# Kernel optimization log

Hardware: AMD Instinct MI355X
Metric: run time of the kernel (lower is better)

The kernel has to match this reference:

```python
import jax, jax.numpy as jnp
import numpy as np

CLASSES = 21
IOU_THRESH = 0.5
ALPHA = 0.25   # focal loss alpha
GAMMA = 2.0    # focal loss gamma
SL1_BETA = 1.0 # torch SmoothL1Loss default beta
CLS_W = 1.0
REG_W = 1.0
NUM_ANCHORS = 98304
NUM_TARGETS = 1024


def _compute_iou(boxes_a, boxes_b):
    # boxes_a: [T,4], boxes_b: [A,4] in (x1,y1,x2,y2) -> [T,A]
    lt = jnp.maximum(boxes_a[:, None, :2], boxes_b[None, :, :2])
    rb = jnp.minimum(boxes_a[:, None, 2:], boxes_b[None, :, 2:])
    wh = jnp.clip(rb - lt, 0.0)
    inter = wh[..., 0] * wh[..., 1]
    area_a = (boxes_a[:, 2] - boxes_a[:, 0]) * (boxes_a[:, 3] - boxes_a[:, 1])
    area_b = (boxes_b[:, 2] - boxes_b[:, 0]) * (boxes_b[:, 3] - boxes_b[:, 1])
    union = area_a[:, None] + area_b[None, :] - inter
    return inter / jnp.maximum(union, 1e-8)


def _encode(boxes, anchors):
    bw = boxes[:, 2] - boxes[:, 0]
    bh = boxes[:, 3] - boxes[:, 1]
    bcx = boxes[:, 0] + 0.5 * bw
    bcy = boxes[:, 1] + 0.5 * bh
    aw = anchors[:, 2] - anchors[:, 0]
    ah = anchors[:, 3] - anchors[:, 1]
    acx = anchors[:, 0] + 0.5 * aw
    acy = anchors[:, 1] + 0.5 * ah
    tx = (bcx - acx) / aw
    ty = (bcy - acy) / ah
    tw = jnp.log(jnp.maximum(bw, 1e-8) / aw)
    th = jnp.log(jnp.maximum(bh, 1e-8) / ah)
    return jnp.stack([tx, ty, tw, th], axis=1)


def _focal_loss(logits, targets):
    # elementwise sigmoid focal loss (no reduction)
    p = jax.nn.sigmoid(logits)
    # numerically stable BCE with logits
    ce = jnp.maximum(logits, 0.0) - logits * targets + jnp.log1p(jnp.exp(-jnp.abs(logits)))
    p_t = p * targets + (1.0 - p) * (1.0 - targets)
    alpha_t = ALPHA * targets + (1.0 - ALPHA) * (1.0 - targets)
    return alpha_t * (1.0 - p_t) ** GAMMA * ce


def _smooth_l1(diff):
    ad = jnp.abs(diff)
    return jnp.where(ad < SL1_BETA, 0.5 * diff * diff / SL1_BETA, ad - 0.5 * SL1_BETA)


def setup_inputs() -> dict:
    key = jax.random.key(0)
    kA, kW, kT, kJ, kL, kC, kB = jax.random.split(key, 7)
    A, T = NUM_ANCHORS, NUM_TARGETS
    centers = jax.random.uniform(kA, (A, 2), minval=0.15, maxval=0.85)
    sizes = jax.random.uniform(kW, (A, 2), minval=0.05, maxval=0.30)
    anchors = jnp.concatenate([centers - 0.5 * sizes, centers + 0.5 * sizes], axis=1)
    # targets = jittered anchors so IoU >= 0.5 matches exist
    idx = jax.random.randint(kT, (T,), 0, A)
    jitter = jax.random.uniform(kJ, (T, 4), minval=-0.01, maxval=0.01)
    target_boxes = anchors[idx] + jitter
    target_labels = jax.random.randint(kL, (T,), 0, CLASSES)
    classification_preds = jax.random.normal(kC, (A, CLASSES), dtype=jnp.float32)
    boxes_preds = jax.random.normal(kB, (A, 4), dtype=jnp.float32)
    return {
        'classification_preds': classification_preds,
        'boxes_preds': boxes_preds,
        'anchors': anchors,
        'target_boxes': target_boxes,
        'target_labels': target_labels,
    }


def reference(classification_preds, boxes_preds, anchors, target_boxes, target_labels):
    iou = _compute_iou(target_boxes, anchors)  # [T, A]

    # anchor-side matching -> classification targets
    max_iou_for_anchors = jnp.max(iou, axis=0)          # [A]
    target_ids_for_anchors = jnp.argmax(iou, axis=0)     # [A]
    positive_mask = max_iou_for_anchors >= IOU_THRESH    # [A] bool
    n_pos = jnp.sum(positive_mask.astype(jnp.float32))
    onehot = jax.nn.one_hot(target_labels[target_ids_for_anchors], CLASSES, dtype=jnp.float32)
    cls_targets = jnp.where(positive_mask[:, None], onehot, 0.0)
    cls_loss = jnp.sum(_focal_loss(classification_preds, cls_targets)) / n_pos

    max_iou_for_targets = jnp.max(iou, axis=1)          # [T]
    anchor_ids_for_targets = jnp.argmax(iou, axis=1)     # [T]
    t_mask = (max_iou_for_targets >= IOU_THRESH).astype(jnp.float32)  # [T]
    matched_anchors = anchors[anchor_ids_for_targets]    # [T,4]
    encoded = _encode(target_boxes, matched_anchors)     # [T,4]
    pred = boxes_preds[anchor_ids_for_targets]           # [T,4]
    diff = (pred - encoded) * t_mask[:, None]
    n_match = jnp.maximum(jnp.sum(t_mask), 1.0)
    reg_loss = jnp.sum(_smooth_l1(diff)) / (n_match * 4.0)  # mean over matched elements

    w_cls = cls_loss * CLS_W
    w_reg = reg_loss * REG_W
    return (w_cls + w_reg, w_cls, w_reg)
```

## Files before the change

### kernel.cpp

```cpp
#include <hip/hip_runtime.h>
#include <stdint.h>

#define NA 98304
#define NT 1024
#define NC 21
#define ACH 192
#define TCH 8
#define NBLK (ACH * TCH)
#define EPB  256
#define HI_MIN 0xBF000000u


__device__ __forceinline__ float f0(float x) {
    const float ax = fabsf(x);
    const float u  = __expf(-ax);
    const float ce = fmaxf(x, 0.f) + __logf(1.f + u);
    const float p  = (x >= 0.f ? 1.f : u) / (1.f + u);
    return 0.75f * p * p * ce;
}
__device__ __forceinline__ float f1(float x) {
    const float ax = fabsf(x);
    const float u  = __expf(-ax);
    const float ce = fmaxf(x, 0.f) - x + __logf(1.f + u);
    const float p  = (x >= 0.f ? 1.f : u) / (1.f + u);
    const float q  = 1.f - p;
    return 0.25f * q * q * ce;
}
__device__ __forceinline__ unsigned long long mk_key(float iou, unsigned int idx) {
    return ((unsigned long long)(__float_as_uint(iou) | 0x80000000u) << 32) |
           (unsigned long long)(0xFFFFFFFFu - idx);
}
__device__ __forceinline__ float smooth_l1(float d) {
    const float ad = fabsf(d);
    return (ad < 1.f) ? 0.5f * d * d : ad - 0.5f;
}

__global__ __launch_bounds__(256) void k_match(
    const float4* __restrict__ anchors,
    const float4* __restrict__ tboxes,
    const float4* __restrict__ preds4,
    unsigned long long* __restrict__ akeys,
    unsigned long long* __restrict__ tkeys,
    float* __restrict__ f0_part,
    unsigned* __restrict__ hdr)
{
    __shared__ float4 s_t[128];
    __shared__ unsigned long long s_tk[128];
    __shared__ float s_f[4];

    const int tid   = threadIdx.x;
    const int L     = blockIdx.y * ACH + blockIdx.x;
    const int tbase = blockIdx.y * 128;
    const int a0    = blockIdx.x * 512 + tid;
    const int a1    = a0 + 256;

    if (L == 0 && tid < 160) hdr[tid] = 0u;

    if (tid < 128) {
        s_t[tid]  = tboxes[tbase + tid];
        s_tk[tid] = 0ull;
    }
    const float4 A0 = anchors[a0];
    const float4 A1 = anchors[a1];

    float facc;
    {
        const int pb = L * 336;
        const float4 v0 = preds4[pb + tid];
        facc = (f0(v0.x) + f0(v0.y)) + (f0(v0.z) + f0(v0.w));
        if (tid < 80) {
            const float4 v1 = preds4[pb + 256 + tid];
            facc += (f0(v1.x) + f0(v1.y)) + (f0(v1.z) + f0(v1.w));
        }
    }
    __syncthreads();

    const float ar0 = (A0.z - A0.x) * (A0.w - A0.y);
    const float ar1 = (A1.z - A1.x) * (A1.w - A1.y);

    float b0 = 0.f, b1 = 0.f;
    int   i0 = -1,  i1 = -1;

    #pragma unroll 4
    for (int t = 0; t < 128; ++t) {
        const float4 tb = s_t[t];
        const float sa = (tb.z - tb.x) * (tb.w - tb.y);
        {
            const float lx = fmaxf(A0.x, tb.x);
            const float ly = fmaxf(A0.y, tb.y);
            const float rx = fminf(A0.z, tb.z);
            const float ry = fminf(A0.w, tb.w);
            const float w  = fmaxf(rx - lx, 0.f);
            const float h  = fmaxf(ry - ly, 0.f);
            const float inter = w * h;
            const float uni = (ar0 + sa) - inter;
            if (__builtin_expect(inter + inter >= uni, 0)) {
                const float iou = inter / uni;
                if (iou > b0) { b0 = iou; i0 = t; }
                atomicMax(&s_tk[t], mk_key(iou, (unsigned int)a0));
            }
        }
        {
            const float lx = fmaxf(A1.x, tb.x);
            const float ly = fmaxf(A1.y, tb.y);
            const float rx = fminf(A1.z, tb.z);
            const float ry = fminf(A1.w, tb.w);
            const float w  = fmaxf(rx - lx, 0.f);
            const float h  = fmaxf(ry - ly, 0.f);
            const float inter = w * h;
            const float uni = (ar1 + sa) - inter;
            if (__builtin_expect(inter + inter >= uni, 0)) {
                const float iou = inter / uni;
                if (iou > b1) { b1 = iou; i1 = t; }
                atomicMax(&s_tk[t], mk_key(iou, (unsigned int)a1));
            }
        }
    }

    if (i0 >= 0) atomicMax(&akeys[a0], mk_key(b0, (unsigned int)(tbase + i0)));
    if (i1 >= 0) atomicMax(&akeys[a1], mk_key(b1, (unsigned int)(tbase + i1)));

    for (int o = 32; o > 0; o >>= 1) facc += __shfl_down(facc, o);
    const int lane = tid & 63, wid = tid >> 6;
    if (lane == 0) s_f[wid] = facc;

    __syncthreads();
    if (tid < 128) {
        const unsigned long long tk = s_tk[tid];
        if (tk != 0ull) atomicMax(&tkeys[tbase + tid], tk);
    }
    if (tid == 0) f0_part[L] = s_f[0] + s_f[1] + s_f[2] + s_f[3];
}

__global__ __launch_bounds__(256) void k_epi(
    const float* __restrict__ preds,
    const int* __restrict__ tlabels,
    const float4* __restrict__ anchors,
    const float4* __restrict__ tboxes,
    const float4* __restrict__ bpreds,
    const unsigned long long* __restrict__ akeys,
    const unsigned long long* __restrict__ tkeys,
    const float* __restrict__ f0_part,
    double* __restrict__ loss_part,
    int* __restrict__ n_part,
    int* __restrict__ done,
    float* __restrict__ out)
{
    __shared__ float s_red[4];
    __shared__ int   s_cnt[4];
    __shared__ int   s_flag;
    __shared__ float s_s[4], s_m[4];
    __shared__ double s_dbl[64];
    __shared__ int    s_int[16];

    const int tid = threadIdx.x;
    const int blk = blockIdx.x;
    const int lane = tid & 63, wid = tid >> 6;

    float acc = 0.f;
    int   cnt = 0;
    {
        const int a = blk * 384 + tid;
        const unsigned long long k = akeys[a];
        if ((unsigned int)(k >> 32) >= HI_MIN) {
            cnt = 1;
            const int lab = tlabels[0xFFFFFFFFu - (unsigned int)k];
            acc += f1(preds[a * NC + lab]) - f0(preds[a * NC + lab]);
        }
    }
    if (tid < 128) {
        const int a = blk * 384 + 256 + tid;
        const unsigned long long k = akeys[a];
        if ((unsigned int)(k >> 32) >= HI_MIN) {
            cnt += 1;
            const int lab = tlabels[0xFFFFFFFFu - (unsigned int)k];
            acc += f1(preds[a * NC + lab]) - f0(preds[a * NC + lab]);
        }
    }
    if (tid < 6) acc += f0_part[blk * 6 + tid];

    for (int o = 32; o > 0; o >>= 1) {
        acc += __shfl_down(acc, o);
        cnt += __shfl_down(cnt, o);
    }
    if (lane == 0) { s_red[wid] = acc; s_cnt[wid] = cnt; }
    __syncthreads();
    if (tid == 0) {
        atomicAdd(&loss_part[blk & 63],
                  (double)(s_red[0] + s_red[1] + s_red[2] + s_red[3]));
        atomicAdd(&n_part[blk & 15], s_cnt[0] + s_cnt[1] + s_cnt[2] + s_cnt[3]);
        __threadfence();
        s_flag = (atomicAdd(done, 1) == EPB - 1);
    }
    __syncthreads();
    if (!s_flag) return;

    float s = 0.f, m = 0.f;
    #pragma unroll
    for (int j = 0; j < 4; ++j) {
        const int t = tid + 256 * j;
        const unsigned long long key = tkeys[t];
        if ((unsigned int)(key >> 32) >= HI_MIN) {
            const unsigned int ga = 0xFFFFFFFFu - (unsigned int)key;
            const float4 tb  = tboxes[t];
            const float4 abx = anchors[ga];
            const float4 pb  = bpreds[ga];
            const float bw = tb.z - tb.x, bh = tb.w - tb.y;
            const float bcx = tb.x + 0.5f * bw, bcy = tb.y + 0.5f * bh;
            const float aw = abx.z - abx.x, ah = abx.w - abx.y;
            const float acx = abx.x + 0.5f * aw, acy = abx.y + 0.5f * ah;
            const float tx = (bcx - acx) / aw;
            const float ty = (bcy - acy) / ah;
            const float tw = logf(fmaxf(bw, 1e-8f) / aw);
            const float th = logf(fmaxf(bh, 1e-8f) / ah);
            s += smooth_l1(pb.x - tx) + smooth_l1(pb.y - ty) +
                 smooth_l1(pb.z - tw) + smooth_l1(pb.w - th);
            m += 1.f;
        }
    }
    for (int o = 32; o > 0; o >>= 1) {
        s += __shfl_down(s, o);
        m += __shfl_down(m, o);
    }
    __syncthreads();
    if (lane == 0) { s_s[wid] = s; s_m[wid] = m; }

    if (tid < 64) s_dbl[tid] = atomicAdd(&loss_part[tid], 0.0);
    if (tid >= 64 && tid < 80) s_int[tid - 64] = atomicAdd(&n_part[tid - 64], 0);
    __syncthreads();
    if (tid == 0) {
        double cl = 0.0;
        for (int i = 0; i < 64; ++i) cl += s_dbl[i];
        int np = 0;
        for (int i = 0; i < 16; ++i) np += s_int[i];
        const float rs = s_s[0] + s_s[1] + s_s[2] + s_s[3];
        const float rm = s_m[0] + s_m[1] + s_m[2] + s_m[3];
        const float cls = (float)(cl / (double)np);
        const float reg = rs / (fmaxf(rm, 1.f) * 4.f);
        out[0] = cls + reg;
        out[1] = cls;
        out[2] = reg;
    }
}

extern "C" void kernel_launch(void* const* d_in, const int* in_sizes, int n_in,
                              void* d_out, int out_size, void* d_ws, size_t ws_size,
                              hipStream_t stream) {
    const float*  preds   = (const float*)d_in[0];
    const float4* preds4  = (const float4*)d_in[0];
    const float4* bpreds  = (const float4*)d_in[1];
    const float4* anchors = (const float4*)d_in[2];
    const float4* tboxes  = (const float4*)d_in[3];
    const int*    tlabels = (const int*)d_in[4];

    char* ws = (char*)d_ws;
    int*    done      = (int*)(ws + 0);
    double* loss_part = (double*)(ws + 64);
    int*    n_part    = (int*)(ws + 576);
    float*  f0_part   = (float*)(ws + 1024);
    unsigned long long* tkeys = (unsigned long long*)(ws + 8192);
    unsigned long long* akeys = (unsigned long long*)(ws + 16384);

    k_match<<<dim3(ACH, TCH), 256, 0, stream>>>(anchors, tboxes, preds4,
                                                akeys, tkeys, f0_part,
                                                (unsigned*)d_ws);
    k_epi<<<EPB, 256, 0, stream>>>(preds, tlabels, anchors, tboxes, bpreds,
                                   akeys, tkeys, f0_part, loss_part, n_part,
                                   done, (float*)d_out);
}
```

Before: 138.2 us.

## Fuse matching and epilogue into one kernel with last-block reductions

Merges the separate matching and epilogue kernels into a single launch. The last of the TCH target-chunk blocks for each anchor chunk computes the positive-anchor correction and count. The last of those per-chunk finishers then does the target-side regression and the final reduction. This removes a kernel launch and its dependency gap. It adds a hipMemsetAsync to clear the counters, plus atomic reads and fences for cross-block visibility.

```diff
diff --git a/kernel.cpp b/kernel.cpp
--- a/kernel.cpp
+++ b/kernel.cpp
@@ -7,7 +7,6 @@
 #define ACH 192
 #define TCH 8
 #define NBLK (ACH * TCH)
-#define EPB  256
 #define HI_MIN 0xBF000000u
 
 
@@ -35,26 +34,39 @@
     return (ad < 1.f) ? 0.5f * d * d : ad - 0.5f;
 }
 
-__global__ __launch_bounds__(256) void k_match(
+__global__ __launch_bounds__(256) void k_all(
+    const float* __restrict__ preds,
+    const float4* __restrict__ preds4,
+    const int* __restrict__ tlabels,
     const float4* __restrict__ anchors,
     const float4* __restrict__ tboxes,
-    const float4* __restrict__ preds4,
+    const float4* __restrict__ bpreds,
     unsigned long long* __restrict__ akeys,
     unsigned long long* __restrict__ tkeys,
     float* __restrict__ f0_part,
-    unsigned* __restrict__ hdr)
+    float* __restrict__ corr_part,
+    int* __restrict__ npos_part,
+    int* __restrict__ done_ac,
+    int* __restrict__ done2,
+    float* __restrict__ out)
 {
     __shared__ float4 s_t[128];
     __shared__ unsigned long long s_tk[128];
     __shared__ float s_f[4];
+    __shared__ int   s_last, s_fin;
+    __shared__ float s_a[4];
+    __shared__ int   s_c[4];
+    __shared__ double s_d[4];
+    __shared__ int    s_i[4];
+    __shared__ float  s_s[4], s_m[4];
 
     const int tid   = threadIdx.x;
-    const int L     = blockIdx.y * ACH + blockIdx.x;
+    const int ac    = blockIdx.x;
+    const int L     = blockIdx.y * ACH + ac;
     const int tbase = blockIdx.y * 128;
-    const int a0    = blockIdx.x * 512 + tid;
+    const int a0    = ac * 512 + tid;
     const int a1    = a0 + 256;
-
-    if (L == 0 && tid < 160) hdr[tid] = 0u;
+    const int lane  = tid & 63, wid = tid >> 6;
 
     if (tid < 128) {
         s_t[tid]  = tboxes[tbase + tid];
@@ -121,7 +133,6 @@
     if (i1 >= 0) atomicMax(&akeys[a1], mk_key(b1, (unsigned int)(tbase + i1)));
 
     for (int o = 32; o > 0; o >>= 1) facc += __shfl_down(facc, o);
-    const int lane = tid & 63, wid = tid >> 6;
     if (lane == 0) s_f[wid] = facc;
 
     __syncthreads();
@@ -129,77 +140,65 @@
         const unsigned long long tk = s_tk[tid];
         if (tk != 0ull) atomicMax(&tkeys[tbase + tid], tk);
     }
-    if (tid == 0) f0_part[L] = s_f[0] + s_f[1] + s_f[2] + s_f[3];
-}
-
-__global__ __launch_bounds__(256) void k_epi(
-    const float* __restrict__ preds,
-    const int* __restrict__ tlabels,
-    const float4* __restrict__ anchors,
-    const float4* __restrict__ tboxes,
-    const float4* __restrict__ bpreds,
-    const unsigned long long* __restrict__ akeys,
-    const unsigned long long* __restrict__ tkeys,
-    const float* __restrict__ f0_part,
-    double* __restrict__ loss_part,
-    int* __restrict__ n_part,
-    int* __restrict__ done,
-    float* __restrict__ out)
-{
-    __shared__ float s_red[4];
-    __shared__ int   s_cnt[4];
-    __shared__ int   s_flag;
-    __shared__ float s_s[4], s_m[4];
-    __shared__ double s_dbl[64];
-    __shared__ int    s_int[16];
-
-    const int tid = threadIdx.x;
-    const int blk = blockIdx.x;
-    const int lane = tid & 63, wid = tid >> 6;
+    if (tid == 0)
+        atomicExch(&f0_part[L], s_f[0] + s_f[1] + s_f[2] + s_f[3]);
+
+    __syncthreads();
+    if (tid == 0) {
+        __threadfence();
+        s_last = (atomicAdd(&done_ac[ac], 1) == TCH - 1);
+    }
+    __syncthreads();
+    if (!s_last) return;
 
     float acc = 0.f;
     int   cnt = 0;
     {
-        const int a = blk * 384 + tid;
-        const unsigned long long k = akeys[a];
+        const unsigned long long k = atomicMax(&akeys[a0], 0ull);
         if ((unsigned int)(k >> 32) >= HI_MIN) {
             cnt = 1;
             const int lab = tlabels[0xFFFFFFFFu - (unsigned int)k];
-            acc += f1(preds[a * NC + lab]) - f0(preds[a * NC + lab]);
-        }
-    }
-    if (tid < 128) {
-        const int a = blk * 384 + 256 + tid;
-        const unsigned long long k = akeys[a];
+            const float x = preds[a0 * NC + lab];
+            acc += f1(x) - f0(x);
+        }
+    }
+    {
+        const unsigned long long k = atomicMax(&akeys[a1], 0ull);
         if ((unsigned int)(k >> 32) >= HI_MIN) {
             cnt += 1;
             const int lab = tlabels[0xFFFFFFFFu - (unsigned int)k];
-            acc += f1(preds[a * NC + lab]) - f0(preds[a * NC + lab]);
-        }
-    }
-    if (tid < 6) acc += f0_part[blk * 6 + tid];
+            const float x = preds[a1 * NC + lab];
+            acc += f1(x) - f0(x);
+        }
+    }
+    if (tid < TCH) acc += atomicAdd(&f0_part[ac + tid * ACH], 0.f);
 
     for (int o = 32; o > 0; o >>= 1) {
         acc += __shfl_down(acc, o);
         cnt += __shfl_down(cnt, o);
     }
-    if (lane == 0) { s_red[wid] = acc; s_cnt[wid] = cnt; }
+    if (lane == 0) { s_a[wid] = acc; s_c[wid] = cnt; }
     __syncthreads();
     if (tid == 0) {
-        atomicAdd(&loss_part[blk & 63],
-                  (double)(s_red[0] + s_red[1] + s_red[2] + s_red[3]));
-        atomicAdd(&n_part[blk & 15], s_cnt[0] + s_cnt[1] + s_cnt[2] + s_cnt[3]);
+        atomicExch(&corr_part[ac], s_a[0] + s_a[1] + s_a[2] + s_a[3]);
+        atomicExch(&npos_part[ac], s_c[0] + s_c[1] + s_c[2] + s_c[3]);
         __threadfence();
-        s_flag = (atomicAdd(done, 1) == EPB - 1);
-    }
-    __syncthreads();
-    if (!s_flag) return;
-
+        s_fin = (atomicAdd(done2, 1) == ACH - 1);
+    }
+    __syncthreads();
+    if (!s_fin) return;
+
+    double cl = 0.0;
+    int    np = 0;
+    if (tid < ACH) {
+        cl = (double)atomicAdd(&corr_part[tid], 0.f);
+        np = atomicAdd(&npos_part[tid], 0);
+    }
     float s = 0.f, m = 0.f;
     #pragma unroll
     for (int j = 0; j < 4; ++j) {
         const int t = tid + 256 * j;
-        const unsigned long long key = tkeys[t];
+        const unsigned long long key = atomicMax(&tkeys[t], 0ull);
         if ((unsigned int)(key >> 32) >= HI_MIN) {
             const unsigned int ga = 0xFFFFFFFFu - (unsigned int)key;
             const float4 tb  = tboxes[t];
@@ -219,23 +218,20 @@
         }
     }
     for (int o = 32; o > 0; o >>= 1) {
-        s += __shfl_down(s, o);
-        m += __shfl_down(m, o);
-    }
-    __syncthreads();
-    if (lane == 0) { s_s[wid] = s; s_m[wid] = m; }
-
-    if (tid < 64) s_dbl[tid] = atomicAdd(&loss_part[tid], 0.0);
-    if (tid >= 64 && tid < 80) s_int[tid - 64] = atomicAdd(&n_part[tid - 64], 0);
+        cl += __shfl_down(cl, o);
+        np += __shfl_down(np, o);
+        s  += __shfl_down(s, o);
+        m  += __shfl_down(m, o);
+    }
+    __syncthreads();
+    if (lane == 0) { s_d[wid] = cl; s_i[wid] = np; s_s[wid] = s; s_m[wid] = m; }
     __syncthreads();
     if (tid == 0) {
-        double cl = 0.0;
-        for (int i = 0; i < 64; ++i) cl += s_dbl[i];
-        int np = 0;
-        for (int i = 0; i < 16; ++i) np += s_int[i];
-        const float rs = s_s[0] + s_s[1] + s_s[2] + s_s[3];
-        const float rm = s_m[0] + s_m[1] + s_m[2] + s_m[3];
-        const float cls = (float)(cl / (double)np);
+        const double cls_sum = s_d[0] + s_d[1] + s_d[2] + s_d[3];
+        const int    npos    = s_i[0] + s_i[1] + s_i[2] + s_i[3];
+        const float  rs      = s_s[0] + s_s[1] + s_s[2] + s_s[3];
+        const float  rm      = s_m[0] + s_m[1] + s_m[2] + s_m[3];
+        const float cls = (float)(cls_sum / (double)npos);
         const float reg = rs / (fmaxf(rm, 1.f) * 4.f);
         out[0] = cls + reg;
         out[1] = cls;
@@ -254,17 +250,18 @@
     const int*    tlabels = (const int*)d_in[4];
 
     char* ws = (char*)d_ws;
-    int*    done      = (int*)(ws + 0);
-    double* loss_part = (double*)(ws + 64);
-    int*    n_part    = (int*)(ws + 576);
+    int*    done2     = (int*)(ws + 0);
+    int*    done_ac   = (int*)(ws + 64);
     float*  f0_part   = (float*)(ws + 1024);
-    unsigned long long* tkeys = (unsigned long long*)(ws + 8192);
-    unsigned long long* akeys = (unsigned long long*)(ws + 16384);
-
-    k_match<<<dim3(ACH, TCH), 256, 0, stream>>>(anchors, tboxes, preds4,
-                                                akeys, tkeys, f0_part,
-                                                (unsigned*)d_ws);
-    k_epi<<<EPB, 256, 0, stream>>>(preds, tlabels, anchors, tboxes, bpreds,
-                                   akeys, tkeys, f0_part, loss_part, n_part,
-                                   done, (float*)d_out);
-}
+    float*  corr_part = (float*)(ws + 7168);
+    int*    npos_part = (int*)(ws + 7936);
+    unsigned long long* tkeys = (unsigned long long*)(ws + 12288);
+    unsigned long long* akeys = (unsigned long long*)(ws + 20480);
+
+    hipMemsetAsync(d_ws, 0, 1024, stream);
+
+    k_all<<<dim3(ACH, TCH), 256, 0, stream>>>(
+        preds, preds4, tlabels, anchors, tboxes, bpreds,
+        akeys, tkeys, f0_part, corr_part, npos_part,
+        done_ac, done2, (float*)d_out);
+}
```

After: 137.5 us, median of 2. No clear change (-0.5%).
